# Kernel tuning notes

Hardware: AMD Instinct MI355X
Metric: run time of the kernel (lower is better)

## Reference

```python
import jax, jax.numpy as jnp
import numpy as np

N, E, C = 100000, 500000, 128
LN_EPS = 1e-5


def setup_inputs() -> dict:
    key = jax.random.key(0)
    ks = jax.random.split(key, 6)
    x = jax.random.normal(ks[0], (N, C), dtype=jnp.float32)
    edge_index = jax.random.randint(ks[1], (2, E), 0, N, dtype=jnp.int32)
    edge_weight = jax.random.uniform(ks[2], (E,), dtype=jnp.float32)
    scale = 1.0 / np.sqrt(C)
    W1 = jax.random.normal(ks[3], (C, C), dtype=jnp.float32) * scale
    W2 = jax.random.normal(ks[4], (C, C), dtype=jnp.float32) * scale
    b1 = jnp.zeros((C,), jnp.float32)
    b2 = jnp.zeros((C,), jnp.float32)
    g1 = jnp.ones((C,), jnp.float32)
    g2 = jnp.ones((C,), jnp.float32)
    beta1 = jnp.zeros((C,), jnp.float32)
    beta2 = jnp.zeros((C,), jnp.float32)
    return {"x": x, "edge_index": edge_index, "edge_weight": edge_weight,
            "W1": W1, "b1": b1, "g1": g1, "beta1": beta1,
            "W2": W2, "b2": b2, "g2": g2, "beta2": beta2}


def _gcn_norm(edge_index, edge_weight, n):
    # add self loops (weight 1.0), then symmetric deg^{-1/2} normalization;
    # degree() in the source counts edges into col (unweighted), incl. self loops
    src = jnp.concatenate([edge_index[0], jnp.arange(n, dtype=edge_index.dtype)])
    dst = jnp.concatenate([edge_index[1], jnp.arange(n, dtype=edge_index.dtype)])
    ew = jnp.concatenate([edge_weight, jnp.ones((n,), edge_weight.dtype)])
    deg = jax.ops.segment_sum(jnp.ones_like(ew), dst, num_segments=n)
    dis = jnp.where(deg > 0, jax.lax.rsqrt(jnp.maximum(deg, 1.0)) * (deg > 0), 0.0)
    w = dis[src] * ew * dis[dst]
    return src, dst, w


def _layernorm(y, g, b):
    mu = jnp.mean(y, axis=-1, keepdims=True)
    var = jnp.mean(jnp.square(y - mu), axis=-1, keepdims=True)
    return (y - mu) * jax.lax.rsqrt(var + LN_EPS) * g + b


def _gcn_layer(x, W, bias, src, dst, w, n):
    h = x @ W                               # [N,C] linear (no bias)
    msg = w[:, None] * h[src]               # gather + edge scaling [E+N,C]
    out = jax.ops.segment_sum(msg, dst, num_segments=n)  # scatter-add
    return out + bias


def reference(x, edge_index, edge_weight, W1, b1, g1, beta1, W2, b2, g2, beta2):
    n = x.shape[0]
    src, dst, w = _gcn_norm(edge_index, edge_weight, n)
    identity = x
    h = _gcn_layer(x, W1, b1, src, dst, w, n)
    h = jax.nn.gelu(_layernorm(h, g1, beta1), approximate=False)
    h = _gcn_layer(h, W2, b2, src, dst, w, n)
    h = jax.nn.gelu(_layernorm(h, g2, beta2), approximate=False)
    return h + identity
```

## Files before the change

kernel.cpp:

```cpp
#include <hip/hip_runtime.h>
#include <math.h>

#define C 128
#define SLOTS 16
#define OVFCAP 8192
#define DSTRIDE 132

typedef __attribute__((ext_vector_type(8))) short short8;
typedef __attribute__((ext_vector_type(4))) float f32x4;
typedef __attribute__((ext_vector_type(2))) float f32x2;
typedef __attribute__((ext_vector_type(8))) unsigned short ushort8_t;

__device__ inline unsigned short f2b(float f) {
    union { float f; unsigned int u; } v; v.f = f;
    unsigned int u = v.u;
    return (unsigned short)((u + 0x7FFFu + ((u >> 16) & 1u)) >> 16);
}
__device__ inline float bits2f(unsigned int u) {
    union { unsigned int u; float f; } v; v.u = u; return v.f;
}
__device__ inline int f2bits(float f) {
    union { float f; int i; } v; v.f = f; return v.i;
}

__device__ inline void acc8(f32x2* a, uint4 u, f32x2 s) {
    f32x2 v0 = {bits2f(u.x << 16), bits2f(u.x & 0xFFFF0000u)};
    f32x2 v1 = {bits2f(u.y << 16), bits2f(u.y & 0xFFFF0000u)};
    f32x2 v2 = {bits2f(u.z << 16), bits2f(u.z & 0xFFFF0000u)};
    f32x2 v3 = {bits2f(u.w << 16), bits2f(u.w & 0xFFFF0000u)};
    a[0] += s * v0;
    a[1] += s * v1;
    a[2] += s * v2;
    a[3] += s * v3;
}

__device__ inline void place_edge(int d, int slot, int s, int wbits,
                                  int2* __restrict__ eslot, int* __restrict__ ovfcnt,
                                  int4* __restrict__ ovf) {
    if (slot < SLOTS) {
        eslot[(size_t)d * SLOTS + slot] = make_int2(s, wbits);
    } else {
        int oi = atomicAdd(ovfcnt, 1);
        if (oi < OVFCAP) ovf[oi] = make_int4(d, s, wbits, 0);
    }
}

__global__ void k_place_cvt(const int* __restrict__ src, const int* __restrict__ dst,
                            const float* __restrict__ ew,
                            int* __restrict__ cnt, int* __restrict__ ovfcnt,
                            int2* __restrict__ eslot, int4* __restrict__ ovf,
                            int e, int bc,
                            const float* __restrict__ x, unsigned short* __restrict__ xb,
                            int ncvt8) {
    const int bid = blockIdx.x;
    const int tid = threadIdx.x;
    if (bid < bc) {
        int i = bid * 256 + tid;
        if (i < ncvt8) {
            const float4* xp = (const float4*)(x + (size_t)i * 8);
            float4 v0 = xp[0];
            float4 v1 = xp[1];
            ushort8_t pkt;
            pkt[0] = f2b(v0.x); pkt[1] = f2b(v0.y); pkt[2] = f2b(v0.z); pkt[3] = f2b(v0.w);
            pkt[4] = f2b(v1.x); pkt[5] = f2b(v1.y); pkt[6] = f2b(v1.z); pkt[7] = f2b(v1.w);
            *(ushort8_t*)(xb + (size_t)i * 8) = pkt;
        }
    } else {
        const int i0 = (bid - bc) * 1024 + tid * 4;
        if (((e & 3) == 0) && (i0 + 3 < e)) {
            int4 s4 = *(const int4*)(src + i0);
            int4 d4 = *(const int4*)(dst + i0);
            float4 w4 = *(const float4*)(ew + i0);
            int sl0 = atomicAdd(&cnt[d4.x], 1);
            int sl1 = atomicAdd(&cnt[d4.y], 1);
            int sl2 = atomicAdd(&cnt[d4.z], 1);
            int sl3 = atomicAdd(&cnt[d4.w], 1);
            place_edge(d4.x, sl0, s4.x, f2bits(w4.x), eslot, ovfcnt, ovf);
            place_edge(d4.y, sl1, s4.y, f2bits(w4.y), eslot, ovfcnt, ovf);
            place_edge(d4.z, sl2, s4.z, f2bits(w4.z), eslot, ovfcnt, ovf);
            place_edge(d4.w, sl3, s4.w, f2bits(w4.w), eslot, ovfcnt, ovf);
        } else {
            #pragma unroll
            for (int k = 0; k < 4; ++k) {
                int i = i0 + k;
                if (i < e) {
                    int s = src[i], d = dst[i];
                    int slot = atomicAdd(&cnt[d], 1);
                    place_edge(d, slot, s, f2bits(ew[i]), eslot, ovfcnt, ovf);
                }
            }
        }
    }
}

__global__ void k_patch_pack(int* __restrict__ cnt, const int* __restrict__ ovfcnt,
                             int2* __restrict__ eslot, int4* __restrict__ ovf,
                             int n, int nslotb,
                             const float* __restrict__ W1, const float* __restrict__ W2,
                             unsigned short* __restrict__ W1p, unsigned short* __restrict__ W2p) {
    const int bid = blockIdx.x;
    const int tid = threadIdx.x;
    if (bid < nslotb) {
        int sidx = bid * 256 + tid;
        if (sidx < n * SLOTS) {
            int d = sidx >> 4, k = sidx & (SLOTS - 1);
            int cd = cnt[d];
            int kend = cd < SLOTS ? cd : SLOTS;
            if (k < kend) {
                int2 ee = eslot[sidx];
                float w = rsqrtf((float)cnt[ee.x] + 1.0f) * bits2f((unsigned int)ee.y)
                        * rsqrtf((float)cd + 1.0f);
                eslot[sidx].y = f2bits(w);
            }
        }
        return;
    }
    int pb = bid - nslotb;
    if (pb < 128) {
        int idx = pb * 256 + tid;
        const float* W = (idx < C * C) ? W1 : W2;
        unsigned short* Wp = (idx < C * C) ? W1p : W2p;
        int p = idx & (C * C - 1);
        int j = p & 7;
        int l = (p >> 3) & 63;
        int t = p >> 9;
        int ks = t & 3, ct = t >> 2;
        int k = ks * 32 + ((l >> 4) << 3) + j;
        int c = (ct << 4) + (l & 15);
        Wp[p] = f2b(W[k * C + c]);
        return;
    }
    int oi = (pb - 128) * 256 + tid;
    int no = *ovfcnt;
    if (no > OVFCAP) no = OVFCAP;
    if (oi < no) {
        int4 ov = ovf[oi];
        float w = rsqrtf((float)cnt[ov.y] + 1.0f) * bits2f((unsigned int)ov.z)
                * rsqrtf((float)cnt[ov.x] + 1.0f);
        ovf[oi].z = f2bits(w);
    }
}

__global__ __launch_bounds__(512) void k_layer(
    const int* __restrict__ cnt, const int* __restrict__ ovfcnt,
    const int2* __restrict__ eslot, const int4* __restrict__ ovf,
    const unsigned short* __restrict__ Xin,
    const unsigned short* __restrict__ Wp,
    const float* __restrict__ bias, const float* __restrict__ g,
    const float* __restrict__ beta,
    const unsigned short* __restrict__ xb_resid,
    unsigned short* __restrict__ out_bf16, float* __restrict__ out_f32, int n) {
    __shared__ int2 eds[32 * SLOTS];
    __shared__ unsigned short xs[32 * C];
    __shared__ float dacc[32 * DSTRIDE];
    const int tid = threadIdx.x;
    const int lane = tid & 63;
    const int wid = tid >> 6;
    const int grp = lane >> 4;
    const int sub = lane & 15;
    const int base = blockIdx.x * 32;
    const int c0 = sub * 8;

    {
        size_t gi = (size_t)base * SLOTS + tid;
        eds[tid] = (gi < (size_t)n * SLOTS) ? eslot[gi] : make_int2(0, 0);
    }
    __syncthreads();

    {
        int r = wid * 4 + grp;
        int row = base + r;
        f32x2 a[4] = {f32x2{0.f, 0.f}, f32x2{0.f, 0.f}, f32x2{0.f, 0.f}, f32x2{0.f, 0.f}};
        if (row < n) {
            int cd = cnt[row];
            float disr = rsqrtf((float)cd + 1.0f);
            {
                f32x2 d2 = {disr * disr, disr * disr};
                uint4 hu = *(const uint4*)(Xin + (size_t)row * C + c0);
                acc8(a, hu, d2);
            }
            const int kb = r * SLOTS;
            const int ke = kb + (cd < SLOTS ? cd : SLOTS);
            int k = kb;
            for (; k + 3 < ke; k += 4) {
                int2 e0 = eds[k];
                int2 e1 = eds[k + 1];
                int2 e2 = eds[k + 2];
                int2 e3 = eds[k + 3];
                uint4 u0 = *(const uint4*)(Xin + (size_t)e0.x * C + c0);
                uint4 u1 = *(const uint4*)(Xin + (size_t)e1.x * C + c0);
                uint4 u2 = *(const uint4*)(Xin + (size_t)e2.x * C + c0);
                uint4 u3 = *(const uint4*)(Xin + (size_t)e3.x * C + c0);
                float w0 = bits2f((unsigned int)e0.y);
                float w1 = bits2f((unsigned int)e1.y);
                float w2 = bits2f((unsigned int)e2.y);
                float w3 = bits2f((unsigned int)e3.y);
                acc8(a, u0, f32x2{w0, w0});
                acc8(a, u1, f32x2{w1, w1});
                acc8(a, u2, f32x2{w2, w2});
                acc8(a, u3, f32x2{w3, w3});
            }
            for (; k < ke; ++k) {
                int2 e0 = eds[k];
                uint4 u0 = *(const uint4*)(Xin + (size_t)e0.x * C + c0);
                float w0 = bits2f((unsigned int)e0.y);
                acc8(a, u0, f32x2{w0, w0});
            }
            int no = *ovfcnt;
            if (no > 0) {
                if (no > OVFCAP) no = OVFCAP;
                for (int oi = 0; oi < no; ++oi) {
                    int4 ov = ovf[oi];
                    if (ov.x == row) {
                        uint4 u0 = *(const uint4*)(Xin + (size_t)ov.y * C + c0);
                        float w0 = bits2f((unsigned int)ov.z);
                        acc8(a, u0, f32x2{w0, w0});
                    }
                }
            }
        }
        ushort8_t pkt;
        #pragma unroll
        for (int q = 0; q < 4; ++q) { pkt[q * 2] = f2b(a[q].x); pkt[q * 2 + 1] = f2b(a[q].y); }
        int byte = (r * 256 + c0 * 2) ^ ((r & 7) << 4);
        *(ushort8_t*)((char*)xs + byte) = pkt;
    }
    __syncthreads();

    {
        const int wm = wid >> 2;
        const int wn = wid & 3;
        const int arow = wm * 16 + (lane & 15);
        const int kg = lane >> 4;

        f32x4 acc[2] = {f32x4{0, 0, 0, 0}, f32x4{0, 0, 0, 0}};

        #pragma unroll
        for (int ks = 0; ks < 4; ++ks) {
            int abyte = (arow * 256 + ks * 64 + kg * 16) ^ ((arow & 7) << 4);
            short8 av = *(const short8*)((const char*)xs + abyte);
            #pragma unroll
            for (int nt = 0; nt < 2; ++nt) {
                int ct = wn * 2 + nt;
                short8 bv = *(const short8*)(Wp + (size_t)((ct * 4 + ks) * 64 + lane) * 8);
                acc[nt] = __builtin_amdgcn_mfma_f32_16x16x32_bf16(av, bv, acc[nt], 0, 0, 0);
            }
        }

        const int rb = wm * 16 + kg * 4;
        #pragma unroll
        for (int nt = 0; nt < 2; ++nt) {
            int col = wn * 32 + nt * 16 + (lane & 15);
            float bv = bias[col];
            #pragma unroll
            for (int r2 = 0; r2 < 4; ++r2)
                dacc[(rb + r2) * DSTRIDE + col] = acc[nt][r2] + bv;
        }
    }
    __syncthreads();

    {
        int r = wid * 4 + grp;
        int row = base + r;
        if (row >= n) return;

        const float* dp = dacc + r * DSTRIDE + c0;
        float4 v0 = *(const float4*)(dp);
        float4 v1 = *(const float4*)(dp + 4);
        float a[8] = {v0.x, v0.y, v0.z, v0.w, v1.x, v1.y, v1.z, v1.w};

        float s = 0.f, sq = 0.f;
        #pragma unroll
        for (int j = 0; j < 8; ++j) { s += a[j]; sq += a[j] * a[j]; }
        #pragma unroll
        for (int off = 8; off >= 1; off >>= 1) {
            s  += __shfl_xor(s, off, 64);
            sq += __shfl_xor(sq, off, 64);
        }
        float mu = s * (1.0f / C);
        float var = sq * (1.0f / C) - mu * mu;
        float rstd = rsqrtf(var + 1e-5f);

        float4 gv0 = *(const float4*)(g + c0);
        float4 gv1 = *(const float4*)(g + c0 + 4);
        float4 be0 = *(const float4*)(beta + c0);
        float4 be1 = *(const float4*)(beta + c0 + 4);
        float gg[8] = {gv0.x, gv0.y, gv0.z, gv0.w, gv1.x, gv1.y, gv1.z, gv1.w};
        float bb[8] = {be0.x, be0.y, be0.z, be0.w, be1.x, be1.y, be1.z, be1.w};

        float t[8];
        #pragma unroll
        for (int j = 0; j < 8; ++j) {
            float v = (a[j] - mu) * rstd * gg[j] + bb[j];
            t[j] = 0.5f * v * (1.0f + erff(v * 0.70710678118654752f));
        }

        if (out_f32 != nullptr) {
            ushort8_t rv = *(const ushort8_t*)(xb_resid + (size_t)row * C + c0);
            #pragma unroll
            for (int j = 0; j < 8; ++j)
                t[j] += bits2f(((unsigned int)(unsigned short)rv[j]) << 16);
            *(float4*)(out_f32 + (size_t)row * C + c0) = make_float4(t[0], t[1], t[2], t[3]);
            *(float4*)(out_f32 + (size_t)row * C + c0 + 4) = make_float4(t[4], t[5], t[6], t[7]);
        } else {
            ushort8_t pkt;
            #pragma unroll
            for (int j = 0; j < 8; ++j) pkt[j] = f2b(t[j]);
            *(ushort8_t*)(out_bf16 + (size_t)row * C + c0) = pkt;
        }
    }
}


extern "C" void kernel_launch(void* const* d_in, const int* in_sizes, int n_in,
                              void* d_out, int out_size, void* d_ws, size_t ws_size,
                              hipStream_t stream) {
    const float* x      = (const float*)d_in[0];
    const int*   eidx   = (const int*)d_in[1];
    const float* ew     = (const float*)d_in[2];
    const float* W1     = (const float*)d_in[3];
    const float* b1     = (const float*)d_in[4];
    const float* g1     = (const float*)d_in[5];
    const float* beta1  = (const float*)d_in[6];
    const float* W2     = (const float*)d_in[7];
    const float* b2     = (const float*)d_in[8];
    const float* g2     = (const float*)d_in[9];
    const float* beta2  = (const float*)d_in[10];

    const int n = in_sizes[0] / C;
    const int e = in_sizes[2];
    const int* src = eidx;
    const int* dst = eidx + e;

    float* out = (float*)d_out;

    char* p = (char*)d_ws;
    auto alloc = [&](size_t bytes) {
        char* q = p;
        p += (bytes + 255) & ~(size_t)255;
        return q;
    };
    int*   cnt    = (int*)alloc(sizeof(int) * (n + 1));
    int2*  eslot  = (int2*)alloc(sizeof(int2) * (size_t)n * SLOTS);
    int4*  ovf    = (int4*)alloc(sizeof(int4) * OVFCAP);
    unsigned short* xb    = (unsigned short*)alloc(sizeof(unsigned short) * (size_t)n * C);
    unsigned short* hact1 = (unsigned short*)alloc(sizeof(unsigned short) * (size_t)n * C);
    unsigned short* W1p   = (unsigned short*)alloc(sizeof(unsigned short) * C * C);
    unsigned short* W2p   = (unsigned short*)alloc(sizeof(unsigned short) * C * C);
    int* ovfcnt = cnt + n;

    const int B = 256;
    const int ge4 = (e + 1023) / 1024;
    const int ncvt8 = n * C / 8;
    const int bc = (ncvt8 + B - 1) / B;
    const int nslotb = (n * SLOTS + B - 1) / B;

    hipMemsetAsync(cnt, 0, sizeof(int) * (n + 1), stream);
    k_place_cvt<<<bc + ge4, B, 0, stream>>>(src, dst, ew, cnt, ovfcnt, eslot, ovf,
                                            e, bc, x, xb, ncvt8);
    k_patch_pack<<<nslotb + 128 + OVFCAP / B, B, 0, stream>>>(cnt, ovfcnt, eslot, ovf,
                                                              n, nslotb, W1, W2, W1p, W2p);

    k_layer<<<(n + 31) / 32, 512, 0, stream>>>(cnt, ovfcnt, eslot, ovf, xb, W1p,
                                               b1, g1, beta1, nullptr,
                                               hact1, nullptr, n);

    k_layer<<<(n + 31) / 32, 512, 0, stream>>>(cnt, ovfcnt, eslot, ovf, hact1, W2p,
                                               b2, g2, beta2, xb,
                                               nullptr, out, n);
}
```

Before: 143.8 us.

## Compute GCN edge norms on the fly and drop the patch kernel

Removes the separate patch kernel that rewrote each slotted and overflow edge weight with the symmetric degree normalization. Each layer kernel now reads the source node's count and computes the normalized weight itself. Weight packing and x-to-bf16 conversion move into the edge placement kernel, so the prep stage is one launch instead of two. The trade is an extra random gather of cnt[src] plus an rsqrt per edge in both layers, in exchange for one fewer launch and one fewer full pass over the slot array.

Result: faster. 138.5 us (median of 2 runs) (-3.7%).

```diff
diff --git a/kernel.cpp b/kernel.cpp
--- a/kernel.cpp
+++ b/kernel.cpp
@@ -45,28 +45,20 @@
     }
 }
 
-__global__ void k_place_cvt(const int* __restrict__ src, const int* __restrict__ dst,
-                            const float* __restrict__ ew,
-                            int* __restrict__ cnt, int* __restrict__ ovfcnt,
-                            int2* __restrict__ eslot, int4* __restrict__ ovf,
-                            int e, int bc,
-                            const float* __restrict__ x, unsigned short* __restrict__ xb,
-                            int ncvt8) {
+__global__ void k_place_cvt_pack(const int* __restrict__ src, const int* __restrict__ dst,
+                                 const float* __restrict__ ew,
+                                 int* __restrict__ cnt, int* __restrict__ ovfcnt,
+                                 int2* __restrict__ eslot, int4* __restrict__ ovf,
+                                 int e, int ge4,
+                                 const float* __restrict__ x, unsigned short* __restrict__ xb,
+                                 int ncvt8,
+                                 const float* __restrict__ W1, const float* __restrict__ W2,
+                                 unsigned short* __restrict__ W1p,
+                                 unsigned short* __restrict__ W2p) {
     const int bid = blockIdx.x;
     const int tid = threadIdx.x;
-    if (bid < bc) {
-        int i = bid * 256 + tid;
-        if (i < ncvt8) {
-            const float4* xp = (const float4*)(x + (size_t)i * 8);
-            float4 v0 = xp[0];
-            float4 v1 = xp[1];
-            ushort8_t pkt;
-            pkt[0] = f2b(v0.x); pkt[1] = f2b(v0.y); pkt[2] = f2b(v0.z); pkt[3] = f2b(v0.w);
-            pkt[4] = f2b(v1.x); pkt[5] = f2b(v1.y); pkt[6] = f2b(v1.z); pkt[7] = f2b(v1.w);
-            *(ushort8_t*)(xb + (size_t)i * 8) = pkt;
-        }
-    } else {
-        const int i0 = (bid - bc) * 1024 + tid * 4;
+    if (bid < ge4) {
+        const int i0 = bid * 1024 + tid * 4;
         if (((e & 3) == 0) && (i0 + 3 < e)) {
             int4 s4 = *(const int4*)(src + i0);
             int4 d4 = *(const int4*)(dst + i0);
@@ -90,34 +82,10 @@
                 }
             }
         }
-    }
-}
-
-__global__ void k_patch_pack(int* __restrict__ cnt, const int* __restrict__ ovfcnt,
-                             int2* __restrict__ eslot, int4* __restrict__ ovf,
-                             int n, int nslotb,
-                             const float* __restrict__ W1, const float* __restrict__ W2,
-                             unsigned short* __restrict__ W1p, unsigned short* __restrict__ W2p) {
-    const int bid = blockIdx.x;
-    const int tid = threadIdx.x;
-    if (bid < nslotb) {
-        int sidx = bid * 256 + tid;
-        if (sidx < n * SLOTS) {
-            int d = sidx >> 4, k = sidx & (SLOTS - 1);
-            int cd = cnt[d];
-            int kend = cd < SLOTS ? cd : SLOTS;
-            if (k < kend) {
-                int2 ee = eslot[sidx];
-                float w = rsqrtf((float)cnt[ee.x] + 1.0f) * bits2f((unsigned int)ee.y)
-                        * rsqrtf((float)cd + 1.0f);
-                eslot[sidx].y = f2bits(w);
-            }
-        }
         return;
     }
-    int pb = bid - nslotb;
-    if (pb < 128) {
-        int idx = pb * 256 + tid;
+    if (bid < ge4 + 128) {
+        int idx = (bid - ge4) * 256 + tid;
         const float* W = (idx < C * C) ? W1 : W2;
         unsigned short* Wp = (idx < C * C) ? W1p : W2p;
         int p = idx & (C * C - 1);
@@ -130,14 +98,15 @@
         Wp[p] = f2b(W[k * C + c]);
         return;
     }
-    int oi = (pb - 128) * 256 + tid;
-    int no = *ovfcnt;
-    if (no > OVFCAP) no = OVFCAP;
-    if (oi < no) {
-        int4 ov = ovf[oi];
-        float w = rsqrtf((float)cnt[ov.y] + 1.0f) * bits2f((unsigned int)ov.z)
-                * rsqrtf((float)cnt[ov.x] + 1.0f);
-        ovf[oi].z = f2bits(w);
+    int i = (bid - ge4 - 128) * 256 + tid;
+    if (i < ncvt8) {
+        const float4* xp = (const float4*)(x + (size_t)i * 8);
+        float4 v0 = xp[0];
+        float4 v1 = xp[1];
+        ushort8_t pkt;
+        pkt[0] = f2b(v0.x); pkt[1] = f2b(v0.y); pkt[2] = f2b(v0.z); pkt[3] = f2b(v0.w);
+        pkt[4] = f2b(v1.x); pkt[5] = f2b(v1.y); pkt[6] = f2b(v1.z); pkt[7] = f2b(v1.w);
+        *(ushort8_t*)(xb + (size_t)i * 8) = pkt;
     }
 }
 
@@ -187,14 +156,18 @@
                 int2 e1 = eds[k + 1];
                 int2 e2 = eds[k + 2];
                 int2 e3 = eds[k + 3];
+                int cs0 = cnt[e0.x];
+                int cs1 = cnt[e1.x];
+                int cs2 = cnt[e2.x];
+                int cs3 = cnt[e3.x];
                 uint4 u0 = *(const uint4*)(Xin + (size_t)e0.x * C + c0);
                 uint4 u1 = *(const uint4*)(Xin + (size_t)e1.x * C + c0);
                 uint4 u2 = *(const uint4*)(Xin + (size_t)e2.x * C + c0);
                 uint4 u3 = *(const uint4*)(Xin + (size_t)e3.x * C + c0);
-                float w0 = bits2f((unsigned int)e0.y);
-                float w1 = bits2f((unsigned int)e1.y);
-                float w2 = bits2f((unsigned int)e2.y);
-                float w3 = bits2f((unsigned int)e3.y);
+                float w0 = rsqrtf((float)cs0 + 1.0f) * bits2f((unsigned int)e0.y) * disr;
+                float w1 = rsqrtf((float)cs1 + 1.0f) * bits2f((unsigned int)e1.y) * disr;
+                float w2 = rsqrtf((float)cs2 + 1.0f) * bits2f((unsigned int)e2.y) * disr;
+                float w3 = rsqrtf((float)cs3 + 1.0f) * bits2f((unsigned int)e3.y) * disr;
                 acc8(a, u0, f32x2{w0, w0});
                 acc8(a, u1, f32x2{w1, w1});
                 acc8(a, u2, f32x2{w2, w2});
@@ -202,8 +175,9 @@
             }
             for (; k < ke; ++k) {
                 int2 e0 = eds[k];
+                int cs0 = cnt[e0.x];
                 uint4 u0 = *(const uint4*)(Xin + (size_t)e0.x * C + c0);
-                float w0 = bits2f((unsigned int)e0.y);
+                float w0 = rsqrtf((float)cs0 + 1.0f) * bits2f((unsigned int)e0.y) * disr;
                 acc8(a, u0, f32x2{w0, w0});
             }
             int no = *ovfcnt;
@@ -213,7 +187,8 @@
                     int4 ov = ovf[oi];
                     if (ov.x == row) {
                         uint4 u0 = *(const uint4*)(Xin + (size_t)ov.y * C + c0);
-                        float w0 = bits2f((unsigned int)ov.z);
+                        float w0 = rsqrtf((float)cnt[ov.y] + 1.0f)
+                                 * bits2f((unsigned int)ov.z) * disr;
                         acc8(a, u0, f32x2{w0, w0});
                     }
                 }
@@ -353,13 +328,12 @@
     const int ge4 = (e + 1023) / 1024;
     const int ncvt8 = n * C / 8;
     const int bc = (ncvt8 + B - 1) / B;
-    const int nslotb = (n * SLOTS + B - 1) / B;
 
     hipMemsetAsync(cnt, 0, sizeof(int) * (n + 1), stream);
-    k_place_cvt<<<bc + ge4, B, 0, stream>>>(src, dst, ew, cnt, ovfcnt, eslot, ovf,
-                                            e, bc, x, xb, ncvt8);
-    k_patch_pack<<<nslotb + 128 + OVFCAP / B, B, 0, stream>>>(cnt, ovfcnt, eslot, ovf,
-                                                              n, nslotb, W1, W2, W1p, W2p);
+    k_place_cvt_pack<<<ge4 + 128 + bc, B, 0, stream>>>(src, dst, ew, cnt, ovfcnt,
+                                                       eslot, ovf, e, ge4,
+                                                       x, xb, ncvt8,
+                                                       W1, W2, W1p, W2p);
 
     k_layer<<<(n + 31) / 32, 512, 0, stream>>>(cnt, ovfcnt, eslot, ovf, xb, W1p,
                                                b1, g1, beta1, nullptr,
```
